# Optimization experiments

Hardware: AMD Instinct MI355X
Metric: run time of the kernel (lower is better)

Reference implementation:

```python
import jax, jax.numpy as jnp
import numpy as np

N_NODES = 50000
N_EDGES = 800000
D_IN = 256
D_HID = 128


def setup_inputs() -> dict:
    key = jax.random.key(0)
    ks = jax.random.split(key, 10)
    x = jax.random.normal(ks[0], (N_NODES, D_IN), dtype=jnp.float32)
    edge_index = jax.random.randint(ks[1], (2, N_EDGES), 0, N_NODES, dtype=jnp.int64)
    # GCNConv params (glorot-ish init), 3 layers: 256->128, 128->128, 128->128
    def glorot(k, fan_in, fan_out):
        s = jnp.sqrt(6.0 / (fan_in + fan_out))
        return jax.random.uniform(k, (fan_in, fan_out), jnp.float32, -s, s)
    W0 = glorot(ks[2], D_IN, D_HID)
    b0 = jnp.zeros((D_HID,), jnp.float32)
    W1 = glorot(ks[3], D_HID, D_HID)
    b1 = jnp.zeros((D_HID,), jnp.float32)
    W2 = glorot(ks[4], D_HID, D_HID)
    b2 = jnp.zeros((D_HID,), jnp.float32)
    return {"x": x, "edge_index": edge_index, "W0": W0, "b0": b0,
            "W1": W1, "b1": b1, "W2": W2, "b2": b2}


def _gcn_conv(x, W, b, src, dst, deg_inv_sqrt, deg_inv):
    # PyG GCNConv: x' = D^{-1/2} (A + I) D^{-1/2} (x W) + b
    h = x @ W  # [N, d_out]
    norm = deg_inv_sqrt[src] * deg_inv_sqrt[dst]  # [E]
    msg = h[src] * norm[:, None]  # gather + scale, [E, d_out]
    agg = jax.ops.segment_sum(msg, dst, num_segments=x.shape[0])
    # self-loop contribution: norm = deg^{-1/2} * deg^{-1/2} = 1/deg
    return agg + h * deg_inv[:, None] + b


def reference(x, edge_index, W0, b0, W1, b1, W2, b2):
    src, dst = edge_index[0], edge_index[1]
    n = x.shape[0]
    # degree with self loops (computed on destination, source_to_target flow)
    deg = jax.ops.segment_sum(jnp.ones((src.shape[0],), x.dtype), dst,
                              num_segments=n) + 1.0
    deg_inv_sqrt = deg ** -0.5
    deg_inv = 1.0 / deg
    h = jax.nn.relu(_gcn_conv(x, W0, b0, src, dst, deg_inv_sqrt, deg_inv))
    h = jax.nn.relu(_gcn_conv(h, W1, b1, src, dst, deg_inv_sqrt, deg_inv))
    h = jax.nn.relu(_gcn_conv(h, W2, b2, src, dst, deg_inv_sqrt, deg_inv))
    return h
```

## Files before the change

### kernel.cpp

```cpp
#include <hip/hip_runtime.h>

#define N_NODES 50000
#define N_EDGES 800000
#define D_HID   128

typedef unsigned int uint;
typedef unsigned short ushort;
typedef __attribute__((ext_vector_type(8))) short short8;
typedef __attribute__((ext_vector_type(4))) float f32x4;

#define NB       196
#define CAP      6144
#define P1_BLOCKS 200
#define P1_CHUNK  4000

__global__ __launch_bounds__(256) void part_k(const int* __restrict__ src,
                                              const int* __restrict__ dst,
                                              int* __restrict__ bcur,
                                              int2* __restrict__ ebuf, int e) {
    __shared__ int hist[NB];
    __shared__ int base[NB];
    int tid = threadIdx.x;
    if (tid < NB) hist[tid] = 0;
    __syncthreads();

    int e0 = blockIdx.x * P1_CHUNK;
    int2 ed[16];
    bool val[16];
#pragma unroll
    for (int i = 0; i < 16; ++i) {
        int o = i * 256 + tid;
        int idx = e0 + o;
        val[i] = (o < P1_CHUNK) && (idx < e);
        if (val[i]) {
            ed[i] = make_int2(src[idx], dst[idx]);
            atomicAdd(&hist[ed[i].y >> 8], 1);
        }
    }
    __syncthreads();
    if (tid < NB && hist[tid] > 0) base[tid] = atomicAdd(&bcur[tid], hist[tid]);
    __syncthreads();
    if (tid < NB) hist[tid] = 0;
    __syncthreads();
#pragma unroll
    for (int i = 0; i < 16; ++i) {
        if (val[i]) {
            int bk = ed[i].y >> 8;
            int o  = base[bk] + atomicAdd(&hist[bk], 1);
            if (o < CAP) ebuf[(size_t)bk * CAP + o] = ed[i];
        }
    }
}

__global__ void bscan196_k(const int* __restrict__ bcur, int* __restrict__ boff,
                           int* __restrict__ row_ptr_end) {
    __shared__ int s[256];
    int t = threadIdx.x;
    int v = (t < NB) ? bcur[t] : 0;
    s[t] = v;
    __syncthreads();
    for (int off = 1; off < 256; off <<= 1) {
        int u = (t >= off) ? s[t - off] : 0;
        __syncthreads();
        s[t] += u;
        __syncthreads();
    }
    if (t < NB) boff[t] = s[t] - v;
    if (t == 255) *row_ptr_end = s[255];
}

__global__ __launch_bounds__(256) void csr2_k(const int2* __restrict__ ebuf,
                                              const int* __restrict__ bcnt,
                                              const int* __restrict__ boff,
                                              int* __restrict__ row_ptr,
                                              float* __restrict__ dis,
                                              int* __restrict__ col, int n) {
    __shared__ int deg[256];
    __shared__ int loc[256];
    __shared__ int cur[256];
    __shared__ int win[CAP];
    int b = blockIdx.x, tid = threadIdx.x;
    deg[tid] = 0; cur[tid] = 0;
    __syncthreads();
    int m = bcnt[b]; if (m > CAP) m = CAP;
    const int2* eb = ebuf + (size_t)b * CAP;
    for (int i = tid; i < m; i += 256)
        atomicAdd(&deg[eb[i].y & 255], 1);
    __syncthreads();
    int v = deg[tid];
    loc[tid] = v;
    __syncthreads();
    for (int off = 1; off < 256; off <<= 1) {
        int u = (tid >= off) ? loc[tid - off] : 0;
        __syncthreads();
        loc[tid] += u;
        __syncthreads();
    }
    int excl = loc[tid] - v;
    int node = b * 256 + tid;
    if (node < n) {
        row_ptr[node] = boff[b] + excl;
        dis[node] = rsqrtf((float)v + 1.0f);
    }
    loc[tid] = excl;
    __syncthreads();
    for (int i = tid; i < m; i += 256) {
        int2 ed = eb[i];
        int ll = ed.y & 255;
        int pos = loc[ll] + atomicAdd(&cur[ll], 1);
        win[pos] = ed.x << 8;
    }
    __syncthreads();
    int base0 = boff[b];
    for (int i = tid; i < m; i += 256) col[base0 + i] = win[i];
}

__global__ __launch_bounds__(256) void rowsort_k(const int* __restrict__ rp,
                                                 int* __restrict__ col, int n) {
    int node = blockIdx.x * 4 + (threadIdx.x >> 6);
    if (node >= n) return;
    int lane = threadIdx.x & 63;
    int beg = rp[node], end = rp[node + 1];
    int len = end - beg;
    if (len <= 1) return;
    if (len <= 64) {
        int v = (lane < len) ? col[beg + lane] : 0x7fffffff;
#pragma unroll
        for (int k = 2; k <= 64; k <<= 1)
#pragma unroll
            for (int j = k >> 1; j > 0; j >>= 1) {
                int other = __shfl_xor(v, j);
                bool up    = (lane & k) == 0;
                bool small = (lane & j) == 0;
                v = (small == up) ? min(v, other) : max(v, other);
            }
        if (lane < len) col[beg + lane] = v;
    } else if (lane == 0) {
        for (int i = beg + 1; i < end; ++i) {
            int key = col[i]; int j = i - 1;
            while (j >= beg && col[j] > key) { col[j + 1] = col[j]; --j; }
            col[j + 1] = key;
        }
    }
}

__device__ inline ushort f2bf(float f) {
    unsigned u = __float_as_uint(f);
    unsigned rounding = 0x7fffu + ((u >> 16) & 1u);
    return (ushort)((u + rounding) >> 16);
}
__device__ inline float bf_lo(uint v) { return __uint_as_float(v << 16); }
__device__ inline float bf_hi(uint v) { return __uint_as_float(v & 0xffff0000u); }
__device__ inline short8 cvt8(float4 f0, float4 f1) {
    short8 r;
    r[0] = (short)f2bf(f0.x); r[1] = (short)f2bf(f0.y);
    r[2] = (short)f2bf(f0.z); r[3] = (short)f2bf(f0.w);
    r[4] = (short)f2bf(f1.x); r[5] = (short)f2bf(f1.y);
    r[6] = (short)f2bf(f1.z); r[7] = (short)f2bf(f1.w);
    return r;
}

__device__ inline void gload16(const void* g, void* l) {
    __builtin_amdgcn_global_load_lds(
        (const __attribute__((address_space(1))) uint*)g,
        (__attribute__((address_space(3))) uint*)l, 16, 0, 0);
}

__global__ void wtrans_all_k(const float* __restrict__ W0, const float* __restrict__ W1,
                             const float* __restrict__ W2, ushort* __restrict__ Wt0,
                             ushort* __restrict__ Wt1, ushort* __restrict__ Wt2,
                             uint* __restrict__ hb_padrow) {
    int i = blockIdx.x * 256 + threadIdx.x;
    if (i < 64) hb_padrow[i] = 0;
    const float* W; ushort* Wt; int K, j;
    if (i < 32768)      { W = W0; Wt = Wt0; K = 256; j = i; }
    else if (i < 49152) { W = W1; Wt = Wt1; K = 128; j = i - 32768; }
    else                { W = W2; Wt = Wt2; K = 128; j = i - 49152; }
    int k = j >> 7, n = j & 127;
    Wt[(size_t)n * K + k] = f2bf(W[j]);
}

template<int K, int ROWS, bool AF32>
__global__ __launch_bounds__(256) void gemm_lds_k(const void* __restrict__ Ap,
                                                  const ushort* __restrict__ Bt,
                                                  const float* __restrict__ dis,
                                                  ushort* __restrict__ H,
                                                  int M) {
    constexpr int T  = K / 32;
    constexpr int EB = AF32 ? 4 : 2;
    constexpr int RS = K * EB;
    constexpr int NI = (ROWS * RS) / 4096;
    __shared__ char As[ROWS * RS];

    int tid = threadIdx.x;
    int w = tid >> 6, l = tid & 63, lr = l & 15, hi = l >> 4;
    int cBase = w * 32;

    short8 b[2][T];
#pragma unroll
    for (int c = 0; c < 2; ++c)
#pragma unroll
        for (int t = 0; t < T; ++t)
            b[c][t] = *(const short8*)&Bt[(size_t)(cBase + c * 16 + lr) * K + t * 32 + hi * 8];

    int r0 = blockIdx.x * ROWS;
    const char* gbase = (const char*)Ap + (size_t)r0 * RS;

#pragma unroll
    for (int i = 0; i < NI; ++i) {
        int L0  = (i * 4 + w) * 1024;
        int L   = L0 + l * 16;
        int row = L / RS;
        int cb  = (L % RS) >> 4;
        int gb  = (cb ^ (row & 7)) << 4;
        int grow = (r0 + row < M) ? row : 0;
        gload16(gbase + (size_t)grow * RS + gb, &As[L0]);
    }
    __syncthreads();

    f32x4 acc[ROWS / 16][2];
#pragma unroll
    for (int rb = 0; rb < ROWS / 16; ++rb)
#pragma unroll
        for (int c = 0; c < 2; ++c) acc[rb][c] = (f32x4){0.f, 0.f, 0.f, 0.f};

#pragma unroll
    for (int rb = 0; rb < ROWS / 16; ++rb) {
        int row = rb * 16 + lr;
        int s = row & 7;
        const char* rbase = &As[row * RS];
#pragma unroll
        for (int t = 0; t < T; ++t) {
            short8 a;
            if constexpr (AF32) {
                int cb0 = t * 8 + hi * 2;
                float4 f0 = *(const float4*)(rbase + ((cb0 ^ s) << 4));
                float4 f1 = *(const float4*)(rbase + (((cb0 + 1) ^ s) << 4));
                a = cvt8(f0, f1);
            } else {
                int cb0 = t * 4 + hi;
                a = *(const short8*)(rbase + ((cb0 ^ s) << 4));
            }
#pragma unroll
            for (int c = 0; c < 2; ++c)
                acc[rb][c] = __builtin_amdgcn_mfma_f32_16x16x32_bf16(a, b[c][t], acc[rb][c], 0, 0, 0);
        }
    }

#pragma unroll
    for (int rb = 0; rb < ROWS / 16; ++rb) {
#pragma unroll
        for (int j = 0; j < 4; ++j) {
            int r = r0 + rb * 16 + hi * 4 + j;
            if (r < M) {
                float d = dis[r];
#pragma unroll
                for (int c = 0; c < 2; ++c)
                    H[(size_t)r * 128 + cBase + c * 16 + lr] = f2bf(acc[rb][c][j] * d);
            }
        }
    }
}

template<bool LAST>
__global__ __launch_bounds__(256) void aggregate_k(const ushort* __restrict__ hs,
                                                   const int* __restrict__ row_ptr,
                                                   const int* __restrict__ col,
                                                   const float* __restrict__ dis,
                                                   const float* __restrict__ bias,
                                                   ushort* __restrict__ act,
                                                   float* __restrict__ out,
                                                   int n, int halfG) {
    int bid  = blockIdx.x;
    int half = (bid >= halfG) ? 1 : 0;
    int nb   = bid - half * halfG;
    int node = nb * 4 + (threadIdx.x >> 6);
    if (node >= n) return;
    int lane = threadIdx.x & 63;
    int g  = lane >> 3;
    int cl = lane & 7;
    const char* base = (const char*)hs + half * 128 + (cl << 4);

    float ax[8];
#pragma unroll
    for (int j = 0; j < 8; ++j) ax[j] = 0.f;

    int beg = row_ptr[node], end = row_ptr[node + 1];
    for (int e = beg; e < end; e += 32) {
        int s[4];
#pragma unroll
        for (int q = 0; q < 4; ++q) {
            int idx = e + q * 8 + g;
            s[q] = (idx < end) ? col[idx] : (N_NODES << 8);
        }
        uint4 u[4];
#pragma unroll
        for (int q = 0; q < 4; ++q)
            u[q] = *(const uint4*)(base + (size_t)(uint)s[q]);
#pragma unroll
        for (int q = 0; q < 4; ++q) {
            ax[0] += bf_lo(u[q].x); ax[1] += bf_hi(u[q].x);
            ax[2] += bf_lo(u[q].y); ax[3] += bf_hi(u[q].y);
            ax[4] += bf_lo(u[q].z); ax[5] += bf_hi(u[q].z);
            ax[6] += bf_lo(u[q].w); ax[7] += bf_hi(u[q].w);
        }
    }
#pragma unroll
    for (int j = 0; j < 8; ++j) {
        ax[j] += __shfl_xor(ax[j], 8);
        ax[j] += __shfl_xor(ax[j], 16);
        ax[j] += __shfl_xor(ax[j], 32);
    }
    if (g == 0) {
        float dn = dis[node];
        uint4 un = *(const uint4*)(base + ((size_t)node << 8));
        float hsn[8] = {bf_lo(un.x), bf_hi(un.x), bf_lo(un.y), bf_hi(un.y),
                        bf_lo(un.z), bf_hi(un.z), bf_lo(un.w), bf_hi(un.w)};
        int c0 = half * 64 + cl * 8;
        float4 bv0 = *(const float4*)&bias[c0];
        float4 bv1 = *(const float4*)&bias[c0 + 4];
        float bb[8] = {bv0.x, bv0.y, bv0.z, bv0.w, bv1.x, bv1.y, bv1.z, bv1.w};
        float o[8];
#pragma unroll
        for (int j = 0; j < 8; ++j)
            o[j] = fmaxf((ax[j] + hsn[j]) * dn + bb[j], 0.f);
        if (LAST) {
            *(float4*)&out[(size_t)node * D_HID + c0]     = make_float4(o[0], o[1], o[2], o[3]);
            *(float4*)&out[(size_t)node * D_HID + c0 + 4] = make_float4(o[4], o[5], o[6], o[7]);
        } else {
            uint4 p;
            p.x = (uint)f2bf(o[0]) | ((uint)f2bf(o[1]) << 16);
            p.y = (uint)f2bf(o[2]) | ((uint)f2bf(o[3]) << 16);
            p.z = (uint)f2bf(o[4]) | ((uint)f2bf(o[5]) << 16);
            p.w = (uint)f2bf(o[6]) | ((uint)f2bf(o[7]) << 16);
            *(uint4*)((char*)act + ((size_t)node << 8) + half * 128 + (cl << 4)) = p;
        }
    }
}

extern "C" void kernel_launch(void* const* d_in, const int* in_sizes, int n_in,
                              void* d_out, int out_size, void* d_ws, size_t ws_size,
                              hipStream_t stream) {
    const float* x  = (const float*)d_in[0];
    const int*   ei = (const int*)d_in[1];
    const float* W0 = (const float*)d_in[2];
    const float* b0 = (const float*)d_in[3];
    const float* W1 = (const float*)d_in[4];
    const float* b1 = (const float*)d_in[5];
    const float* W2 = (const float*)d_in[6];
    const float* b2 = (const float*)d_in[7];
    float* out = (float*)d_out;

    const int N = N_NODES, E = N_EDGES;
    const int* src = ei;
    const int* dst = ei + E;

    char* w = (char*)d_ws;
    size_t off = 0;
    auto alloc = [&](size_t bytes) {
        size_t o = off;
        off += (bytes + 255) & ~(size_t)255;
        return o;
    };
    int*    bcur   = (int*)(w + alloc((size_t)NB * 4));
    float*  dis    = (float*)(w + alloc((size_t)N * 4));
    int*    rp     = (int*)(w + alloc((size_t)(N + 1) * 4));
    int*    boff   = (int*)(w + alloc((size_t)NB * 4));
    int*    col    = (int*)(w + alloc((size_t)E * 4));
    int2*   ebuf   = (int2*)(w + alloc((size_t)NB * CAP * 8));
    ushort* hb     = (ushort*)(w + alloc((size_t)(N + 1) * D_HID * 2));
    ushort* act    = (ushort*)(w + alloc((size_t)N * D_HID * 2));
    ushort* Wt0    = (ushort*)(w + alloc((size_t)128 * 256 * 2));
    ushort* Wt1    = (ushort*)(w + alloc((size_t)128 * 128 * 2));
    ushort* Wt2    = (ushort*)(w + alloc((size_t)128 * 128 * 2));
    (void)ws_size; (void)n_in; (void)in_sizes; (void)out_size;

    hipMemsetAsync(bcur, 0, (size_t)NB * 4, stream);

    part_k<<<P1_BLOCKS, 256, 0, stream>>>(src, dst, bcur, ebuf, E);
    bscan196_k<<<1, 256, 0, stream>>>(bcur, boff, rp + N);
    csr2_k<<<NB, 256, 0, stream>>>(ebuf, bcur, boff, rp, dis, col, N);
    rowsort_k<<<(N + 3) / 4, 256, 0, stream>>>(rp, col, N);

    wtrans_all_k<<<256, 256, 0, stream>>>(W0, W1, W2, Wt0, Wt1, Wt2,
                                          (uint*)(hb + (size_t)N * D_HID));

    int g32 = (N + 31) / 32;
    int g64 = (N + 63) / 64;
    int halfG = (N + 3) / 4;
    int agg_grid = 2 * halfG;

    gemm_lds_k<256, 32, true><<<g32, 256, 0, stream>>>(x, Wt0, dis, hb, N);
    aggregate_k<false><<<agg_grid, 256, 0, stream>>>(hb, rp, col, dis, b0, act, out, N, halfG);
    gemm_lds_k<128, 64, false><<<g64, 256, 0, stream>>>(act, Wt1, dis, hb, N);
    aggregate_k<false><<<agg_grid, 256, 0, stream>>>(hb, rp, col, dis, b1, act, out, N, halfG);
    gemm_lds_k<128, 64, false><<<g64, 256, 0, stream>>>(act, Wt2, dis, hb, N);
    aggregate_k<true><<<agg_grid, 256, 0, stream>>>(hb, rp, col, dis, b2, act, out, N, halfG);
}
```

Baseline: 230.7 us.

## Switch aggregation to padded 32-slot ELL layout with overflow fallback path

Builds a fixed-width 32-slot neighbour table per node (padded with a dummy row) while constructing the CSR, then sorts each slot row with a 32-lane bitonic network. The aggregation kernel now does a single fixed-size gather per node, without reading row_ptr or looping. Nodes with more than 32 neighbours are recorded in an overflow list, sorted in CSR form and re-aggregated by a small separate kernel that overwrites their results. This removes variable-length loop and bounds overhead. In exchange it costs extra padded gathers, a 6.4 MB table write, three extra launches, and an overflow cap of 1024 nodes beyond which results would be wrong.

```diff
diff --git a/kernel.cpp b/kernel.cpp
--- a/kernel.cpp
+++ b/kernel.cpp
@@ -3,6 +3,7 @@
 #define N_NODES 50000
 #define N_EDGES 800000
 #define D_HID   128
+#define PAD_V   (N_NODES << 8)
 
 typedef unsigned int uint;
 typedef unsigned short ushort;
@@ -13,6 +14,7 @@
 #define CAP      6144
 #define P1_BLOCKS 200
 #define P1_CHUNK  4000
+#define OVF_CAP  1024
 
 __global__ __launch_bounds__(256) void part_k(const int* __restrict__ src,
                                               const int* __restrict__ dst,
@@ -74,12 +76,16 @@
                                               const int* __restrict__ boff,
                                               int* __restrict__ row_ptr,
                                               float* __restrict__ dis,
-                                              int* __restrict__ col, int n) {
+                                              int* __restrict__ col,
+                                              int* __restrict__ col32,
+                                              int* __restrict__ ovf,
+                                              int* __restrict__ ovf_cnt, int n) {
     __shared__ int deg[256];
     __shared__ int loc[256];
     __shared__ int cur[256];
     __shared__ int win[CAP];
     int b = blockIdx.x, tid = threadIdx.x;
+    int node0 = b * 256;
     deg[tid] = 0; cur[tid] = 0;
     __syncthreads();
     int m = bcnt[b]; if (m > CAP) m = CAP;
@@ -97,10 +103,14 @@
         __syncthreads();
     }
     int excl = loc[tid] - v;
-    int node = b * 256 + tid;
+    int node = node0 + tid;
     if (node < n) {
         row_ptr[node] = boff[b] + excl;
         dis[node] = rsqrtf((float)v + 1.0f);
+        if (v > 32) {
+            int ix = atomicAdd(ovf_cnt, 1);
+            if (ix < OVF_CAP) ovf[ix] = node;
+        }
     }
     loc[tid] = excl;
     __syncthreads();
@@ -113,33 +123,49 @@
     __syncthreads();
     int base0 = boff[b];
     for (int i = tid; i < m; i += 256) col[base0 + i] = win[i];
-}
-
-__global__ __launch_bounds__(256) void rowsort_k(const int* __restrict__ rp,
-                                                 int* __restrict__ col, int n) {
-    int node = blockIdx.x * 4 + (threadIdx.x >> 6);
-    if (node >= n) return;
-    int lane = threadIdx.x & 63;
-    int beg = rp[node], end = rp[node + 1];
-    int len = end - beg;
-    if (len <= 1) return;
-    if (len <= 64) {
-        int v = (lane < len) ? col[beg + lane] : 0x7fffffff;
-#pragma unroll
-        for (int k = 2; k <= 64; k <<= 1)
+    for (int slot = tid; slot < 256 * 32; slot += 256) {
+        int nl = slot >> 5, s = slot & 31;
+        if (node0 + nl < n) {
+            int d = deg[nl];
+            col32[(size_t)node0 * 32 + slot] = (s < d) ? win[loc[nl] + s] : PAD_V;
+        }
+    }
+}
+
+__global__ __launch_bounds__(256) void rowsort32_k(int* __restrict__ col32,
+                                                   const int* __restrict__ rp,
+                                                   int* __restrict__ col,
+                                                   const int* __restrict__ ovf,
+                                                   const int* __restrict__ ovf_cnt,
+                                                   int n, int nblk) {
+    if ((int)blockIdx.x < nblk) {
+        int lane = threadIdx.x & 63;
+        int sub  = lane >> 5;
+        int l32  = lane & 31;
+        int node = blockIdx.x * 8 + (threadIdx.x >> 6) * 2 + sub;
+        if (node >= n) return;
+        int* wp = col32 + (size_t)node * 32;
+        int v = wp[l32];
+#pragma unroll
+        for (int k = 2; k <= 32; k <<= 1)
 #pragma unroll
             for (int j = k >> 1; j > 0; j >>= 1) {
                 int other = __shfl_xor(v, j);
-                bool up    = (lane & k) == 0;
-                bool small = (lane & j) == 0;
+                bool up    = (l32 & k) == 0;
+                bool small = (l32 & j) == 0;
                 v = (small == up) ? min(v, other) : max(v, other);
             }
-        if (lane < len) col[beg + lane] = v;
-    } else if (lane == 0) {
-        for (int i = beg + 1; i < end; ++i) {
-            int key = col[i]; int j = i - 1;
-            while (j >= beg && col[j] > key) { col[j + 1] = col[j]; --j; }
-            col[j + 1] = key;
+        wp[l32] = v;
+    } else {
+        int cnt = *ovf_cnt; if (cnt > OVF_CAP) cnt = OVF_CAP;
+        for (int i = threadIdx.x; i < cnt; i += 256) {
+            int node = ovf[i];
+            int beg = rp[node], end = rp[node + 1];
+            for (int a = beg + 1; a < end; ++a) {
+                int key = col[a]; int j = a - 1;
+                while (j >= beg && col[j] > key) { col[j + 1] = col[j]; --j; }
+                col[j + 1] = key;
+            }
         }
     }
 }
@@ -264,52 +290,43 @@
 
 template<bool LAST>
 __global__ __launch_bounds__(256) void aggregate_k(const ushort* __restrict__ hs,
-                                                   const int* __restrict__ row_ptr,
-                                                   const int* __restrict__ col,
+                                                   const int* __restrict__ col32,
                                                    const float* __restrict__ dis,
                                                    const float* __restrict__ bias,
                                                    ushort* __restrict__ act,
-                                                   float* __restrict__ out,
-                                                   int n, int halfG) {
+                                                   float* __restrict__ out, int halfG) {
     int bid  = blockIdx.x;
     int half = (bid >= halfG) ? 1 : 0;
-    int nb   = bid - half * halfG;
-    int node = nb * 4 + (threadIdx.x >> 6);
-    if (node >= n) return;
+    int node = (bid - half * halfG) * 4 + (threadIdx.x >> 6);
     int lane = threadIdx.x & 63;
     int g  = lane >> 3;
     int cl = lane & 7;
     const char* base = (const char*)hs + half * 128 + (cl << 4);
 
-    float ax[8];
-#pragma unroll
-    for (int j = 0; j < 8; ++j) ax[j] = 0.f;
-
-    int beg = row_ptr[node], end = row_ptr[node + 1];
-    for (int e = beg; e < end; e += 32) {
-        int s[4];
-#pragma unroll
-        for (int q = 0; q < 4; ++q) {
-            int idx = e + q * 8 + g;
-            s[q] = (idx < end) ? col[idx] : (N_NODES << 8);
-        }
-        uint4 u[4];
-#pragma unroll
-        for (int q = 0; q < 4; ++q)
-            u[q] = *(const uint4*)(base + (size_t)(uint)s[q]);
-#pragma unroll
-        for (int q = 0; q < 4; ++q) {
-            ax[0] += bf_lo(u[q].x); ax[1] += bf_hi(u[q].x);
-            ax[2] += bf_lo(u[q].y); ax[3] += bf_hi(u[q].y);
-            ax[4] += bf_lo(u[q].z); ax[5] += bf_hi(u[q].z);
-            ax[6] += bf_lo(u[q].w); ax[7] += bf_hi(u[q].w);
-        }
-    }
+    const int* cw = col32 + (size_t)node * 32 + g * 4;
+    int s0 = cw[0], s1 = cw[1], s2 = cw[2], s3 = cw[3];
+    uint4 u0 = *(const uint4*)(base + (size_t)(uint)s0);
+    uint4 u1 = *(const uint4*)(base + (size_t)(uint)s1);
+    uint4 u2 = *(const uint4*)(base + (size_t)(uint)s2);
+    uint4 u3 = *(const uint4*)(base + (size_t)(uint)s3);
+
+    float2 ax[4];
+#pragma unroll
+    for (int i = 0; i < 4; ++i) ax[i] = make_float2(0.f, 0.f);
+    uint4 uu[4] = {u0, u1, u2, u3};
+#pragma unroll
+    for (int q = 0; q < 4; ++q) {
+        ax[0].x += bf_lo(uu[q].x); ax[0].y += bf_hi(uu[q].x);
+        ax[1].x += bf_lo(uu[q].y); ax[1].y += bf_hi(uu[q].y);
+        ax[2].x += bf_lo(uu[q].z); ax[2].y += bf_hi(uu[q].z);
+        ax[3].x += bf_lo(uu[q].w); ax[3].y += bf_hi(uu[q].w);
+    }
+    float o[8] = {ax[0].x, ax[0].y, ax[1].x, ax[1].y, ax[2].x, ax[2].y, ax[3].x, ax[3].y};
 #pragma unroll
     for (int j = 0; j < 8; ++j) {
-        ax[j] += __shfl_xor(ax[j], 8);
-        ax[j] += __shfl_xor(ax[j], 16);
-        ax[j] += __shfl_xor(ax[j], 32);
+        o[j] += __shfl_xor(o[j], 8);
+        o[j] += __shfl_xor(o[j], 16);
+        o[j] += __shfl_xor(o[j], 32);
     }
     if (g == 0) {
         float dn = dis[node];
@@ -320,10 +337,9 @@
         float4 bv0 = *(const float4*)&bias[c0];
         float4 bv1 = *(const float4*)&bias[c0 + 4];
         float bb[8] = {bv0.x, bv0.y, bv0.z, bv0.w, bv1.x, bv1.y, bv1.z, bv1.w};
-        float o[8];
 #pragma unroll
         for (int j = 0; j < 8; ++j)
-            o[j] = fmaxf((ax[j] + hsn[j]) * dn + bb[j], 0.f);
+            o[j] = fmaxf((o[j] + hsn[j]) * dn + bb[j], 0.f);
         if (LAST) {
             *(float4*)&out[(size_t)node * D_HID + c0]     = make_float4(o[0], o[1], o[2], o[3]);
             *(float4*)&out[(size_t)node * D_HID + c0 + 4] = make_float4(o[4], o[5], o[6], o[7]);
@@ -334,6 +350,68 @@
             p.z = (uint)f2bf(o[4]) | ((uint)f2bf(o[5]) << 16);
             p.w = (uint)f2bf(o[6]) | ((uint)f2bf(o[7]) << 16);
             *(uint4*)((char*)act + ((size_t)node << 8) + half * 128 + (cl << 4)) = p;
+        }
+    }
+}
+
+template<bool LAST>
+__global__ __launch_bounds__(256) void ovf_agg_k(const ushort* __restrict__ hs,
+                                                 const int* __restrict__ rp,
+                                                 const int* __restrict__ col,
+                                                 const float* __restrict__ dis,
+                                                 const float* __restrict__ bias,
+                                                 ushort* __restrict__ act,
+                                                 float* __restrict__ out,
+                                                 const int* __restrict__ ovf,
+                                                 const int* __restrict__ ovf_cnt) {
+    int cnt = *ovf_cnt; if (cnt > OVF_CAP) cnt = OVF_CAP;
+    int wid = threadIdx.x >> 6, lane = threadIdx.x & 63;
+    int g = lane >> 4, cl = lane & 15;
+    const char* base = (const char*)hs + (cl << 4);
+    for (int i = wid; i < cnt; i += 4) {
+        int node = ovf[i];
+        float ax[8];
+#pragma unroll
+        for (int j = 0; j < 8; ++j) ax[j] = 0.f;
+        int beg = rp[node], end = rp[node + 1];
+        for (int e = beg; e < end; e += 4) {
+            int idx = e + g;
+            int s = (idx < end) ? col[idx] : PAD_V;
+            uint4 u = *(const uint4*)(base + (size_t)(uint)s);
+            ax[0] += bf_lo(u.x); ax[1] += bf_hi(u.x);
+            ax[2] += bf_lo(u.y); ax[3] += bf_hi(u.y);
+            ax[4] += bf_lo(u.z); ax[5] += bf_hi(u.z);
+            ax[6] += bf_lo(u.w); ax[7] += bf_hi(u.w);
+        }
+#pragma unroll
+        for (int j = 0; j < 8; ++j) {
+            ax[j] += __shfl_xor(ax[j], 16);
+            ax[j] += __shfl_xor(ax[j], 32);
+        }
+        if (g == 0) {
+            float dn = dis[node];
+            uint4 un = *(const uint4*)(base + ((size_t)node << 8));
+            float hsn[8] = {bf_lo(un.x), bf_hi(un.x), bf_lo(un.y), bf_hi(un.y),
+                            bf_lo(un.z), bf_hi(un.z), bf_lo(un.w), bf_hi(un.w)};
+            int c0 = cl * 8;
+            float4 bv0 = *(const float4*)&bias[c0];
+            float4 bv1 = *(const float4*)&bias[c0 + 4];
+            float bb[8] = {bv0.x, bv0.y, bv0.z, bv0.w, bv1.x, bv1.y, bv1.z, bv1.w};
+            float o[8];
+#pragma unroll
+            for (int j = 0; j < 8; ++j)
+                o[j] = fmaxf((ax[j] + hsn[j]) * dn + bb[j], 0.f);
+            if (LAST) {
+                *(float4*)&out[(size_t)node * D_HID + c0]     = make_float4(o[0], o[1], o[2], o[3]);
+                *(float4*)&out[(size_t)node * D_HID + c0 + 4] = make_float4(o[4], o[5], o[6], o[7]);
+            } else {
+                uint4 p;
+                p.x = (uint)f2bf(o[0]) | ((uint)f2bf(o[1]) << 16);
+                p.y = (uint)f2bf(o[2]) | ((uint)f2bf(o[3]) << 16);
+                p.z = (uint)f2bf(o[4]) | ((uint)f2bf(o[5]) << 16);
+                p.w = (uint)f2bf(o[6]) | ((uint)f2bf(o[7]) << 16);
+                *(uint4*)((char*)act + ((size_t)node << 8) + (cl << 4)) = p;
+            }
         }
     }
 }
@@ -362,38 +440,45 @@
         off += (bytes + 255) & ~(size_t)255;
         return o;
     };
-    int*    bcur   = (int*)(w + alloc((size_t)NB * 4));
+    int*    bcur   = (int*)(w + alloc((size_t)(NB + 1) * 4));
+    int*    ovf    = (int*)(w + alloc((size_t)OVF_CAP * 4));
     float*  dis    = (float*)(w + alloc((size_t)N * 4));
     int*    rp     = (int*)(w + alloc((size_t)(N + 1) * 4));
     int*    boff   = (int*)(w + alloc((size_t)NB * 4));
     int*    col    = (int*)(w + alloc((size_t)E * 4));
+    int*    col32  = (int*)(w + alloc((size_t)N * 32 * 4));
     int2*   ebuf   = (int2*)(w + alloc((size_t)NB * CAP * 8));
     ushort* hb     = (ushort*)(w + alloc((size_t)(N + 1) * D_HID * 2));
     ushort* act    = (ushort*)(w + alloc((size_t)N * D_HID * 2));
     ushort* Wt0    = (ushort*)(w + alloc((size_t)128 * 256 * 2));
     ushort* Wt1    = (ushort*)(w + alloc((size_t)128 * 128 * 2));
     ushort* Wt2    = (ushort*)(w + alloc((size_t)128 * 128 * 2));
+    int*    ovf_cnt = bcur + NB;
     (void)ws_size; (void)n_in; (void)in_sizes; (void)out_size;
 
-    hipMemsetAsync(bcur, 0, (size_t)NB * 4, stream);
+    hipMemsetAsync(bcur, 0, (size_t)(NB + 1) * 4, stream);
 
     part_k<<<P1_BLOCKS, 256, 0, stream>>>(src, dst, bcur, ebuf, E);
     bscan196_k<<<1, 256, 0, stream>>>(bcur, boff, rp + N);
-    csr2_k<<<NB, 256, 0, stream>>>(ebuf, bcur, boff, rp, dis, col, N);
-    rowsort_k<<<(N + 3) / 4, 256, 0, stream>>>(rp, col, N);
+    csr2_k<<<NB, 256, 0, stream>>>(ebuf, bcur, boff, rp, dis, col, col32, ovf, ovf_cnt, N);
+    int srt_blocks = (N + 7) / 8;
+    rowsort32_k<<<srt_blocks + 1, 256, 0, stream>>>(col32, rp, col, ovf, ovf_cnt, N, srt_blocks);
 
     wtrans_all_k<<<256, 256, 0, stream>>>(W0, W1, W2, Wt0, Wt1, Wt2,
                                           (uint*)(hb + (size_t)N * D_HID));
 
     int g32 = (N + 31) / 32;
     int g64 = (N + 63) / 64;
-    int halfG = (N + 3) / 4;
+    int halfG = N / 4;
     int agg_grid = 2 * halfG;
 
     gemm_lds_k<256, 32, true><<<g32, 256, 0, stream>>>(x, Wt0, dis, hb, N);
-    aggregate_k<false><<<agg_grid, 256, 0, stream>>>(hb, rp, col, dis, b0, act, out, N, halfG);
+    aggregate_k<false><<<agg_grid, 256, 0, stream>>>(hb, col32, dis, b0, act, out, halfG);
+    ovf_agg_k<false><<<1, 256, 0, stream>>>(hb, rp, col, dis, b0, act, out, ovf, ovf_cnt);
     gemm_lds_k<128, 64, false><<<g64, 256, 0, stream>>>(act, Wt1, dis, hb, N);
-    aggregate_k<false><<<agg_grid, 256, 0, stream>>>(hb, rp, col, dis, b1, act, out, N, halfG);
+    aggregate_k<false><<<agg_grid, 256, 0, stream>>>(hb, col32, dis, b1, act, out, halfG);
+    ovf_agg_k<false><<<1, 256, 0, stream>>>(hb, rp, col, dis, b1, act, out, ovf, ovf_cnt);
     gemm_lds_k<128, 64, false><<<g64, 256, 0, stream>>>(act, Wt2, dis, hb, N);
-    aggregate_k<true><<<agg_grid, 256, 0, stream>>>(hb, rp, col, dis, b2, act, out, N, halfG);
-}
+    aggregate_k<true><<<agg_grid, 256, 0, stream>>>(hb, col32, dis, b2, act, out, halfG);
+    ovf_agg_k<true><<<1, 256, 0, stream>>>(hb, rp, col, dis, b2, act, out, ovf, ovf_cnt);
+}
```

Result: slower. 331.7 us (+43.8%).
